# Optimization experiments

Hardware: AMD Instinct MI355X
Metric: run time of the kernel (lower is better)

## Reference

```python
import jax, jax.numpy as jnp
import numpy as np
from itertools import permutations

B, T, A, NIN = 10, 100, 20, 4096
NIMG, NATT, NPHYS = 1024, 512, 256


def _build_perm():
    # all 190 unordered pairs of 20 agents, lexicographically sorted (matches np.unique on sorted perms)
    perm = np.unique(np.sort(np.array(list(permutations(range(A), 2))), axis=1), axis=0)  # (190, 2)
    # for each agent k: the 19 pair-indices containing k, ordered (k in col0 first, then col1) as in torch code
    perm_ind = np.stack([
        np.hstack((np.where(perm[:, 0] == k)[0], np.where(perm[:, 1] == k)[0])) for k in range(A)
    ])  # (20, 19)
    return perm.astype(np.int32), perm_ind.astype(np.int32)

PERM, PERM_IND = _build_perm()


def setup_inputs() -> dict:
    key = jax.random.key(0)
    ks = jax.random.split(key, 7)
    def lin(k, out_f, in_f):
        return (jax.random.normal(k, (out_f, in_f), jnp.float32) / np.float32(np.sqrt(in_f)))
    return {
        "x": jax.random.normal(ks[0], (B, T, A, NIN), jnp.float32),
        "world_coord_feat": jax.random.normal(ks[1], (B, T, A, 13), jnp.float32),
        "W_glob": lin(ks[2], NIMG, NIN), "b_glob": jnp.zeros((NIMG,), jnp.float32),
        "W_loc": lin(ks[3], NATT, NIN), "b_loc": jnp.zeros((NATT,), jnp.float32),
        "W_phys": lin(ks[4], NPHYS, 26), "b_phys": jnp.zeros((NPHYS,), jnp.float32),
        "W_phys3": lin(ks[5], NPHYS, NPHYS), "b_phys3": jnp.zeros((NPHYS,), jnp.float32),
    }


def reference(x, world_coord_feat, W_glob, b_glob, W_loc, b_loc, W_phys, b_phys, W_phys3, b_phys3):
    pa = jnp.asarray(PERM)        # (190, 2)
    pind = jnp.asarray(PERM_IND)  # (20, 19)
    # global / local embeddings
    glob_embed = x[:, :, 0, :] @ W_glob.T + b_glob          # (B, T, NIMG)
    loc_embed = x[:, :, 1:, :] @ W_loc.T + b_loc            # (B, T, 19, NATT)
    # pairwise physical features: concat coords of both agents of each pair
    perm_feat = jnp.concatenate(
        [world_coord_feat[:, :, pa[:, 0], :], world_coord_feat[:, :, pa[:, 1], :]], axis=-1
    )                                                        # (B, T, 190, 26)
    # dropout layers are identity at inference; mask is computed but unused in original
    h1 = jax.nn.relu(perm_feat @ W_phys.T + b_phys)          # (B, T, 190, NPHYS)
    phys = h1 @ W_phys3.T + b_phys3                          # (B, T, 190, NPHYS)
    # per-agent gather of its 19 pairs + max-pool over pairs (fused segment-max)
    agent_tensor = jnp.max(phys[:, :, pind, :], axis=3)      # (B, T, 20, NPHYS)
    return glob_embed, loc_embed, agent_tensor
```

## Files before the change

kernel.cpp:

```cpp
#include <hip/hip_runtime.h>
#include <stdint.h>

typedef __bf16 bf16x8 __attribute__((ext_vector_type(8)));
typedef float  f32x4  __attribute__((ext_vector_type(4)));

__device__ __forceinline__ bf16x8 cvt8(const float* __restrict__ p) {
    float4 lo = *(const float4*)p;
    float4 hi = *(const float4*)(p + 4);
    bf16x8 r;
    r[0] = (__bf16)lo.x; r[1] = (__bf16)lo.y; r[2] = (__bf16)lo.z; r[3] = (__bf16)lo.w;
    r[4] = (__bf16)hi.x; r[5] = (__bf16)hi.y; r[6] = (__bf16)hi.z; r[7] = (__bf16)hi.w;
    return r;
}

__device__ __forceinline__ int pidx(int i, int j) {
    return i * 19 - (i * (i - 1)) / 2 + (j - i - 1);
}

template <int MODE, bool A_BF16, bool OUT_BF16>
__global__ __launch_bounds__(256) void gemm_bias_kernel(
    const void* __restrict__ Xv,
    const float* __restrict__ W,
    const float* __restrict__ bias,
    void* __restrict__ Cv,
    int M, int N, int K)
{
    __shared__ __bf16 As[64][40];
    __shared__ __bf16 Bs[64][40];

    const int tid  = threadIdx.x;
    const int srow = tid >> 2;
    const int scol = (tid & 3) << 3;

    int gmrow = (int)blockIdx.y * 64 + srow;
    int rA = gmrow < M ? gmrow : M - 1;
    size_t aoff;
    if (MODE == 0)      aoff = (size_t)rA * 81920;
    else if (MODE == 1) aoff = ((size_t)(rA / 19) * 20 + (size_t)(rA % 19) + 1) * 4096;
    else                aoff = (size_t)rA * (size_t)K;
    const float*  aptrF = (const float*)Xv  + aoff + scol;
    const __bf16* aptrH = (const __bf16*)Xv + aoff + scol;
    const float*  bptr  = W + (size_t)((int)blockIdx.x * 64 + srow) * (size_t)K + scol;

    const int w    = tid >> 6;
    const int lane = tid & 63;
    const int wm   = (w >> 1) * 32;
    const int wn   = (w & 1) * 32;
    const int l    = lane & 15;
    const int qk   = lane >> 4;
    const int q8   = qk * 8;

    f32x4 acc00 = {}, acc01 = {}, acc10 = {}, acc11 = {};

    for (int k0 = 0; k0 < K; k0 += 32) {
        bf16x8 av, bv;
        if (A_BF16) av = *(const bf16x8*)(aptrH + k0);
        else        av = cvt8(aptrF + k0);
        bv = cvt8(bptr + k0);
        __syncthreads();
        *(bf16x8*)&As[srow][scol] = av;
        *(bf16x8*)&Bs[srow][scol] = bv;
        __syncthreads();
        bf16x8 a0 = *(const bf16x8*)&As[wm + l][q8];
        bf16x8 a1 = *(const bf16x8*)&As[wm + 16 + l][q8];
        bf16x8 b0 = *(const bf16x8*)&Bs[wn + l][q8];
        bf16x8 b1 = *(const bf16x8*)&Bs[wn + 16 + l][q8];
        acc00 = __builtin_amdgcn_mfma_f32_16x16x32_bf16(a0, b0, acc00, 0, 0, 0);
        acc01 = __builtin_amdgcn_mfma_f32_16x16x32_bf16(a0, b1, acc01, 0, 0, 0);
        acc10 = __builtin_amdgcn_mfma_f32_16x16x32_bf16(a1, b0, acc10, 0, 0, 0);
        acc11 = __builtin_amdgcn_mfma_f32_16x16x32_bf16(a1, b1, acc11, 0, 0, 0);
    }

    const int colBase = (int)blockIdx.x * 64;
    const int rowBase = (int)blockIdx.y * 64;
    const float bias0 = bias[colBase + wn + l];
    const float bias1 = bias[colBase + wn + 16 + l];
    #pragma unroll
    for (int i = 0; i < 2; ++i) {
        f32x4 aj0 = (i == 0) ? acc00 : acc10;
        f32x4 aj1 = (i == 0) ? acc01 : acc11;
        #pragma unroll
        for (int r = 0; r < 4; ++r) {
            int row = rowBase + wm + i * 16 + qk * 4 + r;
            if (row < M) {
                size_t base = (size_t)row * (size_t)N + colBase + wn;
                float v0 = aj0[r] + bias0;
                float v1 = aj1[r] + bias1;
                if (OUT_BF16) {
                    ((__bf16*)Cv)[base + l]      = (__bf16)v0;
                    ((__bf16*)Cv)[base + 16 + l] = (__bf16)v1;
                } else {
                    ((float*)Cv)[base + l]      = v0;
                    ((float*)Cv)[base + 16 + l] = v1;
                }
            }
        }
    }
}

__global__ __launch_bounds__(256) void phys1_kernel(
    const float* __restrict__ wcf,
    const float* __restrict__ W1,
    const float* __restrict__ b1,
    __bf16* __restrict__ h1)
{
    __shared__ float fs[260];
    const int g = blockIdx.x;
    const int c = threadIdx.x;
    for (int i = c; i < 260; i += 256) fs[i] = wcf[g * 260 + i];
    float wrow[26];
    #pragma unroll
    for (int k = 0; k < 26; ++k) wrow[k] = W1[c * 26 + k];
    const float bias = b1[c];
    __syncthreads();

    __bf16* out = h1 + (size_t)g * 190 * 256 + c;
    int p = 0;
    for (int i = 0; i < 20; ++i) {
        for (int j = i + 1; j < 20; ++j, ++p) {
            float s = bias;
            #pragma unroll
            for (int k = 0; k < 13; ++k) s += wrow[k]      * fs[i * 13 + k];
            #pragma unroll
            for (int k = 0; k < 13; ++k) s += wrow[13 + k] * fs[j * 13 + k];
            out[(size_t)p * 256] = (__bf16)(s > 0.f ? s : 0.f);
        }
    }
}

__global__ __launch_bounds__(256) void segmax_kernel(
    const __bf16* __restrict__ phys,
    float* __restrict__ agent)
{
    const int a = blockIdx.x;
    const int g = blockIdx.y;
    const int c = threadIdx.x;
    const __bf16* base = phys + (size_t)g * 190 * 256 + c;
    float m = -3.4e38f;
    #pragma unroll
    for (int j = 0; j < 20; ++j) {
        if (j == a) continue;
        int p = (j > a) ? pidx(a, j) : pidx(j, a);
        float v = (float)base[(size_t)p * 256];
        m = v > m ? v : m;
    }
    agent[((size_t)g * 20 + a) * 256 + c] = m;
}

extern "C" void kernel_launch(void* const* d_in, const int* in_sizes, int n_in,
                              void* d_out, int out_size, void* d_ws, size_t ws_size,
                              hipStream_t stream)
{
    const float* x   = (const float*)d_in[0];
    const float* wcf = (const float*)d_in[1];
    const float* Wg  = (const float*)d_in[2];
    const float* bg  = (const float*)d_in[3];
    const float* Wl  = (const float*)d_in[4];
    const float* bl  = (const float*)d_in[5];
    const float* W1  = (const float*)d_in[6];
    const float* b1  = (const float*)d_in[7];
    const float* W3  = (const float*)d_in[8];
    const float* b3  = (const float*)d_in[9];

    float* out   = (float*)d_out;
    float* glob  = out;
    float* loc   = out + 1024000;
    float* agent = out + 1024000 + 9728000;

    __bf16* h1   = (__bf16*)d_ws;
    __bf16* phys = h1 + (size_t)190000 * 256;

    gemm_bias_kernel<0, false, false><<<dim3(1024 / 64, (1000 + 63) / 64), 256, 0, stream>>>(
        x, Wg, bg, glob, 1000, 1024, 4096);
    gemm_bias_kernel<1, false, false><<<dim3(512 / 64, (19000 + 63) / 64), 256, 0, stream>>>(
        x, Wl, bl, loc, 19000, 512, 4096);
    phys1_kernel<<<1000, 256, 0, stream>>>(wcf, W1, b1, h1);
    gemm_bias_kernel<2, true, true><<<dim3(256 / 64, (190000 + 63) / 64), 256, 0, stream>>>(
        h1, W3, b3, phys, 190000, 256, 256);
    segmax_kernel<<<dim3(20, 1000), 256, 0, stream>>>(phys, agent);
}
```

Baseline: 1.037 ms.

## Use 128x128 double-buffered tiled GEMM with XCD-aware block remap for local embedding

Replaces the generic 64x64 GEMM for the local-embedding projection with a dedicated kernel using 128x128 output tiles, a 4x4 MFMA grid per wave, and double-buffered shared memory, with the next K-slice prefetched into registers during compute. Block IDs are remapped so that consecutive tiles land on the same XCD, improving L2 reuse of W and X. This targets the dominant GEMM (19000x512x4096) by increasing arithmetic intensity and hiding global load latency, at the cost of higher register and LDS usage per block, which lowers occupancy.

```diff
diff --git a/kernel.cpp b/kernel.cpp
--- a/kernel.cpp
+++ b/kernel.cpp
@@ -7,6 +7,13 @@
 __device__ __forceinline__ bf16x8 cvt8(const float* __restrict__ p) {
     float4 lo = *(const float4*)p;
     float4 hi = *(const float4*)(p + 4);
+    bf16x8 r;
+    r[0] = (__bf16)lo.x; r[1] = (__bf16)lo.y; r[2] = (__bf16)lo.z; r[3] = (__bf16)lo.w;
+    r[4] = (__bf16)hi.x; r[5] = (__bf16)hi.y; r[6] = (__bf16)hi.z; r[7] = (__bf16)hi.w;
+    return r;
+}
+
+__device__ __forceinline__ bf16x8 pack8(float4 lo, float4 hi) {
     bf16x8 r;
     r[0] = (__bf16)lo.x; r[1] = (__bf16)lo.y; r[2] = (__bf16)lo.z; r[3] = (__bf16)lo.w;
     r[4] = (__bf16)hi.x; r[5] = (__bf16)hi.y; r[6] = (__bf16)hi.z; r[7] = (__bf16)hi.w;
@@ -98,6 +105,112 @@
     }
 }
 
+__global__ __launch_bounds__(256) void gemm_loc_v2(
+    const float* __restrict__ X,
+    const float* __restrict__ W,
+    const float* __restrict__ bias,
+    float* __restrict__ C)
+{
+    constexpr int M = 19000, N = 512, K = 4096;
+    __shared__ __bf16 As[2][128][40];
+    __shared__ __bf16 Bs[2][128][40];
+
+    const int gx = 4, nwg = 596;
+    int lid = (int)blockIdx.y * gx + (int)blockIdx.x;
+    {
+        int q = nwg >> 3, r = nwg & 7;
+        int xcd = lid & 7, idx = lid >> 3;
+        lid = (xcd < r ? xcd * (q + 1) : r * (q + 1) + (xcd - r) * q) + idx;
+    }
+    const int tx = lid % gx;
+    const int ty = lid / gx;
+
+    const int tid  = threadIdx.x;
+    const int srow = tid >> 2;
+    const int scol = (tid & 3) << 3;
+
+    int gr0 = ty * 128 + srow;      int rA0 = gr0 < M ? gr0 : M - 1;
+    int gr1 = gr0 + 64;             int rA1 = gr1 < M ? gr1 : M - 1;
+    const float* aptr0 = X + ((size_t)(rA0 / 19) * 20 + (size_t)(rA0 % 19) + 1) * 4096 + scol;
+    const float* aptr1 = X + ((size_t)(rA1 / 19) * 20 + (size_t)(rA1 % 19) + 1) * 4096 + scol;
+    const float* bptr0 = W + (size_t)(tx * 128 + srow) * (size_t)K + scol;
+    const float* bptr1 = W + (size_t)(tx * 128 + 64 + srow) * (size_t)K + scol;
+
+    const int w    = tid >> 6;
+    const int lane = tid & 63;
+    const int wm   = (w >> 1) * 64;
+    const int wn   = (w & 1) * 64;
+    const int l    = lane & 15;
+    const int qk   = lane >> 4;
+    const int q8   = qk << 3;
+
+    f32x4 acc[4][4];
+    #pragma unroll
+    for (int m = 0; m < 4; ++m)
+        #pragma unroll
+        for (int n = 0; n < 4; ++n) { f32x4 z = {0.f, 0.f, 0.f, 0.f}; acc[m][n] = z; }
+
+    float4 sa0l, sa0h, sa1l, sa1h, sb0l, sb0h, sb1l, sb1h;
+
+    sa0l = *(const float4*)(aptr0);     sa0h = *(const float4*)(aptr0 + 4);
+    sa1l = *(const float4*)(aptr1);     sa1h = *(const float4*)(aptr1 + 4);
+    sb0l = *(const float4*)(bptr0);     sb0h = *(const float4*)(bptr0 + 4);
+    sb1l = *(const float4*)(bptr1);     sb1h = *(const float4*)(bptr1 + 4);
+    *(bf16x8*)&As[0][srow][scol]      = pack8(sa0l, sa0h);
+    *(bf16x8*)&As[0][srow + 64][scol] = pack8(sa1l, sa1h);
+    *(bf16x8*)&Bs[0][srow][scol]      = pack8(sb0l, sb0h);
+    *(bf16x8*)&Bs[0][srow + 64][scol] = pack8(sb1l, sb1h);
+
+    int cur = 0;
+    for (int i = 0; i < K / 32; ++i) {
+        __syncthreads();
+        if (i + 1 < K / 32) {
+            int k0 = (i + 1) << 5;
+            sa0l = *(const float4*)(aptr0 + k0); sa0h = *(const float4*)(aptr0 + k0 + 4);
+            sa1l = *(const float4*)(aptr1 + k0); sa1h = *(const float4*)(aptr1 + k0 + 4);
+            sb0l = *(const float4*)(bptr0 + k0); sb0h = *(const float4*)(bptr0 + k0 + 4);
+            sb1l = *(const float4*)(bptr1 + k0); sb1h = *(const float4*)(bptr1 + k0 + 4);
+        }
+        bf16x8 af[4], bfr[4];
+        #pragma unroll
+        for (int m = 0; m < 4; ++m) af[m]  = *(const bf16x8*)&As[cur][wm + m * 16 + l][q8];
+        #pragma unroll
+        for (int n = 0; n < 4; ++n) bfr[n] = *(const bf16x8*)&Bs[cur][wn + n * 16 + l][q8];
+        #pragma unroll
+        for (int m = 0; m < 4; ++m)
+            #pragma unroll
+            for (int n = 0; n < 4; ++n)
+                acc[m][n] = __builtin_amdgcn_mfma_f32_16x16x32_bf16(af[m], bfr[n], acc[m][n], 0, 0, 0);
+        if (i + 1 < K / 32) {
+            int nb = cur ^ 1;
+            *(bf16x8*)&As[nb][srow][scol]      = pack8(sa0l, sa0h);
+            *(bf16x8*)&As[nb][srow + 64][scol] = pack8(sa1l, sa1h);
+            *(bf16x8*)&Bs[nb][srow][scol]      = pack8(sb0l, sb0h);
+            *(bf16x8*)&Bs[nb][srow + 64][scol] = pack8(sb1l, sb1h);
+        }
+        cur ^= 1;
+    }
+
+    const int colBase = tx * 128 + wn;
+    const int rowBase = ty * 128 + wm;
+    float bs[4];
+    #pragma unroll
+    for (int n = 0; n < 4; ++n) bs[n] = bias[colBase + n * 16 + l];
+    #pragma unroll
+    for (int m = 0; m < 4; ++m) {
+        #pragma unroll
+        for (int r = 0; r < 4; ++r) {
+            int row = rowBase + m * 16 + qk * 4 + r;
+            if (row < M) {
+                size_t base = (size_t)row * (size_t)N + colBase;
+                #pragma unroll
+                for (int n = 0; n < 4; ++n)
+                    C[base + n * 16 + l] = acc[m][n][r] + bs[n];
+            }
+        }
+    }
+}
+
 __global__ __launch_bounds__(256) void phys1_kernel(
     const float* __restrict__ wcf,
     const float* __restrict__ W1,
@@ -172,8 +285,7 @@
 
     gemm_bias_kernel<0, false, false><<<dim3(1024 / 64, (1000 + 63) / 64), 256, 0, stream>>>(
         x, Wg, bg, glob, 1000, 1024, 4096);
-    gemm_bias_kernel<1, false, false><<<dim3(512 / 64, (19000 + 63) / 64), 256, 0, stream>>>(
-        x, Wl, bl, loc, 19000, 512, 4096);
+    gemm_loc_v2<<<dim3(4, 149), 256, 0, stream>>>(x, Wl, bl, loc);
     phys1_kernel<<<1000, 256, 0, stream>>>(wcf, W1, b1, h1);
     gemm_bias_kernel<2, true, true><<<dim3(256 / 64, (190000 + 63) / 64), 256, 0, stream>>>(
         h1, W3, b3, phys, 190000, 256, 256);
```

New measurement: 903.6 us. 12.8% less time.
